# Kernel optimization log

Hardware: AMD Instinct MI355X
Metric: run time of the kernel (lower is better)

The kernel has to match this reference:

```python
import jax, jax.numpy as jnp
import numpy as np

BETA = 0.25

def setup_inputs() -> dict:
    key = jax.random.key(0)
    k1, k2 = jax.random.split(key)
    z_e = jax.random.normal(k1, (32768, 256), dtype=jnp.float32)
    codebook = jax.random.normal(k2, (8192, 256), dtype=jnp.float32)
    return {"z_e": z_e, "codebook": codebook}

def reference(z_e, codebook):
    # Squared distances via ||a||^2 - 2 a.b + ||b||^2 (argmin is invariant to sqrt)
    z_sq = jnp.sum(z_e * z_e, axis=1, keepdims=True)           # (B, 1)
    e_sq = jnp.sum(codebook * codebook, axis=1)                 # (K,)
    cross = jnp.einsum('bd,kd->bk', z_e, codebook)              # (B, K) GEMM
    d2 = z_sq - 2.0 * cross + e_sq[None, :]                     # (B, K)
    indices = jnp.argmin(d2, axis=1)                            # (B,)
    z_q = codebook[indices]                                     # (B, D)
    codebook_loss = jnp.mean((z_q - z_e) ** 2)
    commitment_loss = jnp.mean((z_e - z_q) ** 2)
    vq_loss = codebook_loss + BETA * commitment_loss
    # straight-through value (grad semantics irrelevant in fwd-only)
    z_q_st = z_e + (z_q - z_e)
    return (z_q_st, indices, vq_loss)
```

## Files before the change

kernel.cpp:

```cpp
#include <hip/hip_runtime.h>
#include <hip/hip_bf16.h>
#include <stdint.h>

#define M_ROWS 32768
#define N_CODES 8192
#define K_DIM 256
#define NSLICE 32
#define MARGIN 0.25f
#define MAXCAND 2560

#define BM 256
#define BN 256

typedef _Float16 half8 __attribute__((ext_vector_type(8)));
typedef float f4v __attribute__((ext_vector_type(4)));
typedef float f32x4 __attribute__((ext_vector_type(4)));
typedef __attribute__((address_space(3))) void lds_void;
typedef const __attribute__((address_space(1))) void gbl_cvoid;

__device__ __forceinline__ unsigned mono32(float f) {
    unsigned u = __float_as_uint(f);
    return (u & 0x80000000u) ? ~u : (u | 0x80000000u);
}
__device__ __forceinline__ unsigned long long pack_key(float d, unsigned col) {
    return ((unsigned long long)mono32(d) << 32) | (unsigned long long)col;
}
__device__ __forceinline__ float unpack_key(unsigned long long k) {
    unsigned m = (unsigned)(k >> 32);
    unsigned u = (m & 0x80000000u) ? (m & 0x7fffffffu) : ~m;
    return __uint_as_float(u);
}
__device__ __forceinline__ void merge2(unsigned long long& b1, unsigned long long& b2,
                                       unsigned long long o1, unsigned long long o2) {
    unsigned long long n1 = b1 < o1 ? b1 : o1;
    unsigned long long hi = b1 < o1 ? o1 : b1;
    unsigned long long l2 = b2 < o2 ? b2 : o2;
    b2 = hi < l2 ? hi : l2;
    b1 = n1;
}

__global__ __launch_bounds__(256) void prep_all(const float* __restrict__ z,
                                                const float* __restrict__ cb,
                                                _Float16* __restrict__ Aq,
                                                _Float16* __restrict__ Bq,
                                                float* __restrict__ esq) {
    int b = blockIdx.x;
    if (b < 5120) {
        const float* src = (b < 4096) ? z : cb;
        _Float16* dst = (b < 4096) ? Aq : Bq;
        int e = (b < 4096 ? b : b - 4096) * 256 + threadIdx.x;
        int ln = e & 63, kcg = (e >> 6) & 7, R = e >> 9;
        int row = R * 16 + (ln & 15);
        int k = kcg * 32 + (ln >> 4) * 8;
        const f4v* s4 = (const f4v*)(src + (size_t)row * K_DIM + k);
        f4v v0 = s4[0], v1 = s4[1];
        half8 h;
        #pragma unroll
        for (int j = 0; j < 4; ++j) h[j] = (_Float16)v0[j];
        #pragma unroll
        for (int j = 0; j < 4; ++j) h[4 + j] = (_Float16)v1[j];
        *(half8*)(dst + (size_t)e * 8) = h;
    } else {
        int wave = threadIdx.x >> 6, lane = threadIdx.x & 63;
        int row = (b - 5120) * 4 + wave;
        f4v v = *(const f4v*)(cb + (size_t)row * K_DIM + lane * 4);
        float sq = v[0] * v[0] + v[1] * v[1] + v[2] * v[2] + v[3] * v[3];
        #pragma unroll
        for (int m = 32; m; m >>= 1) sq += __shfl_xor(sq, m);
        if (lane == 0) esq[row] = sq;
    }
}

__global__ __launch_bounds__(512, 2) void coarse_gemm(
        const _Float16* __restrict__ Aq, const _Float16* __restrict__ Bq,
        const float* __restrict__ esq, ulonglong2* __restrict__ slices) {
    __shared__ __align__(16) char smem[131072];
    uint2 (*red)[4] = (uint2(*)[4])smem;

    int bid = blockIdx.x;
    int bn = bid & 31;
    int bm = bid >> 5;
    int m0 = bm * BM, n0 = bn * BN;

    int t = threadIdx.x;
    int lane = t & 63, wave = t >> 6;
    int l15 = lane & 15, quad = lane >> 4;
    int wr = wave >> 2, wc = wave & 3;

    float es_adj[4];
    #pragma unroll
    for (int ni = 0; ni < 4; ++ni)
        es_adj[ni] = esq[n0 + wc * 64 + ni * 16 + l15] + 1024.0f;
    asm volatile("" ::: "memory");

    f32x4 acc[8][4] = {};

    const char* Ab = (const char*)Aq + (size_t)bm * 131072;
    const char* Bb = (const char*)Bq + (size_t)bn * 131072;

    auto stage_half = [&](int ks, int op, int c, char* dstA, char* dstB) {
        const char* gb = op ? Bb : Ab;
        char* db = op ? dstB : dstA;
        #pragma unroll
        for (int i2 = 0; i2 < 2; ++i2) {
            int e = i2 * 512 + t;
            int RB = e >> 6, ln = e & 63;
            __builtin_amdgcn_global_load_lds(
                (gbl_cvoid*)(gb + ((size_t)(RB * 8 + ks * 2 + c) << 10) + ln * 16),
                (lds_void*)(db + ((RB * 2 + c) * 64 + ln) * 16), 16, 0, 0);
        }
    };

    {
        char* A0 = smem, * B0 = smem + 32768;
        stage_half(0, 0, 0, A0, B0);
        stage_half(0, 1, 0, A0, B0);
        stage_half(0, 0, 1, A0, B0);
        stage_half(0, 1, 1, A0, B0);
    }

    half8 bfr[4];
    #pragma unroll
    for (int j = 0; j < 4; ++j) {
        const char* As = smem + (j & 1) * 65536;
        const char* Bs = As + 32768;
        char* Asn = smem + ((j + 1) & 1) * 65536;
        char* Bsn = Asn + 32768;
        #pragma unroll
        for (int p = 0; p < 4; ++p) {
            const int c = p >> 1;
            const int mh = p & 1;
            if (p == 0 || p == 2) {
                if (j == 3 && p == 2)
                    asm volatile("s_waitcnt vmcnt(0)" ::: "memory");
                else
                    asm volatile("s_waitcnt vmcnt(4)" ::: "memory");
                __builtin_amdgcn_s_barrier();
                asm volatile("" ::: "memory");
            }
            half8 afr[4];
            #pragma unroll
            for (int mi = 0; mi < 4; ++mi) {
                int RB = wr * 8 + mh * 4 + mi;
                afr[mi] = *(const half8*)(As + ((RB * 2 + c) * 64 + lane) * 16);
            }
            if (mh == 0) {
                #pragma unroll
                for (int ni = 0; ni < 4; ++ni) {
                    int CB = wc * 4 + ni;
                    bfr[ni] = *(const half8*)(Bs + ((CB * 2 + c) * 64 + lane) * 16);
                }
            }
            if (j < 3) stage_half(j + 1, p & 1, p >> 1, Asn, Bsn);
            __builtin_amdgcn_s_barrier();
            asm volatile("s_waitcnt lgkmcnt(0)" ::: "memory");
            __builtin_amdgcn_sched_barrier(0);
            __builtin_amdgcn_s_setprio(1);
            #pragma unroll
            for (int mi = 0; mi < 4; ++mi)
                #pragma unroll
                for (int ni = 0; ni < 4; ++ni)
                    acc[mh * 4 + mi][ni] = __builtin_amdgcn_mfma_f32_16x16x32_f16(
                        afr[mi], bfr[ni], acc[mh * 4 + mi][ni], 0, 0, 0);
            __builtin_amdgcn_s_setprio(0);
        }
    }

    #pragma unroll
    for (int mi = 0; mi < 8; ++mi) {
        #pragma unroll
        for (int r = 0; r < 4; ++r) {
            unsigned b1 = 0xFFFFFFFFu, b2 = 0xFFFFFFFFu;
            #pragma unroll
            for (int ni = 0; ni < 4; ++ni) {
                float key = fmaf(-2.0f, acc[mi][ni][r], es_adj[ni]);
                unsigned kb = (__float_as_uint(key) & 0xFFFFFFC0u) |
                              (unsigned)(ni * 16 + l15);
                unsigned hi = kb > b1 ? kb : b1;
                b1 = kb < b1 ? kb : b1;
                b2 = hi < b2 ? hi : b2;
            }
            #pragma unroll
            for (int m = 1; m < 16; m <<= 1) {
                unsigned o1 = (unsigned)__shfl_xor((int)b1, m);
                unsigned o2 = (unsigned)__shfl_xor((int)b2, m);
                unsigned hi = b1 > o1 ? b1 : o1;
                b1 = b1 < o1 ? b1 : o1;
                unsigned l2 = b2 < o2 ? b2 : o2;
                b2 = hi < l2 ? hi : l2;
            }
            if (l15 == 0) {
                int rowl = wr * 128 + mi * 16 + quad * 4 + r;
                red[rowl][wc] = make_uint2(b1, b2);
            }
        }
    }
    __syncthreads();
    if (t < 256) {
        unsigned best = 0xFFFFFFFFu, sec = 0xFFFFFFFFu, bq = 0;
        #pragma unroll
        for (int q = 0; q < 4; ++q) {
            uint2 e = red[t][q];
            if (e.x < best) { sec = best; best = e.x; bq = (unsigned)q; }
            else sec = e.x < sec ? e.x : sec;
            sec = e.y < sec ? e.y : sec;
        }
        unsigned col = (unsigned)n0 + bq * 64u + (best & 63u);
        unsigned long long q1 =
            ((unsigned long long)((best & 0xFFFFFFC0u) | 0x80000000u) << 32) | col;
        unsigned long long q2 =
            ((unsigned long long)((sec & 0xFFFFFFC0u) | 0x80000000u) << 32) |
            0xFFFFFFFFull;
        slices[(size_t)(m0 + t) * NSLICE + bn] = make_ulonglong2(q1, q2);
    }
}

__global__ __launch_bounds__(256) void merge_slices(
        const ulonglong2* __restrict__ slices,
        int* __restrict__ bestidx, int* __restrict__ flags,
        int* __restrict__ list, int* __restrict__ count) {
    int t = threadIdx.x;
    int wave = t >> 6, lane = t & 63;
    int half = lane >> 5, idx = lane & 31;
    int row = blockIdx.x * 8 + wave * 2 + half;
    ulonglong2 p = slices[(size_t)row * NSLICE + idx];
    unsigned long long b1 = p.x, b2 = p.y;
    #pragma unroll
    for (int m = 1; m < 32; m <<= 1) {
        unsigned long long o1 = (unsigned long long)__shfl_xor((long long)b1, m);
        unsigned long long o2 = (unsigned long long)__shfl_xor((long long)b2, m);
        merge2(b1, b2, o1, o2);
    }
    if (idx == 0) {
        bestidx[row] = (int)(unsigned)(b1 & 0xFFFFFFFFULL);
        int f = (unpack_key(b2) - unpack_key(b1) <= MARGIN) ? 1 : 0;
        flags[row] = f;
        if (f) { int pos = atomicAdd(count, 1); list[pos] = row; }
    }
}

__global__ __launch_bounds__(256) void refine(
        const float* __restrict__ z, const float* __restrict__ cb,
        const ulonglong2* __restrict__ slices,
        const int* __restrict__ list, const int* __restrict__ count,
        int* __restrict__ bestidx) {
    __shared__ float zrow[K_DIM];
    __shared__ int cand[MAXCAND];
    __shared__ int ncand_s;
    __shared__ unsigned long long sb1;
    __shared__ double wd[4];
    __shared__ int wc[4];
    int t = threadIdx.x, lane = t & 63, wave = t >> 6;
    int n = *count;
    #pragma unroll 1
    for (int li = blockIdx.x; li < n; li += 2048) {
        int row = list[li];
        __syncthreads();
        zrow[t] = z[(size_t)row * K_DIM + t];
        if (t == 0) ncand_s = 0;
        __syncthreads();
        ulonglong2 p = make_ulonglong2(~0ULL, ~0ULL);
        if (wave == 0) {
            if (lane < NSLICE) p = slices[(size_t)row * NSLICE + lane];
            unsigned long long b1 = p.x;
            #pragma unroll
            for (int m = 1; m < 64; m <<= 1) {
                unsigned long long o =
                    (unsigned long long)__shfl_xor((long long)b1, m);
                b1 = o < b1 ? o : b1;
            }
            if (lane == 0) sb1 = b1;
        }
        __syncthreads();
        float thr = unpack_key(sb1) + MARGIN;
        if (wave == 0 && lane < NSLICE) {
            float k1 = unpack_key(p.x), k2 = unpack_key(p.y);
            if (k2 <= thr) {
                int pos = atomicAdd(&ncand_s, 256);
                if (pos + 256 <= MAXCAND)
                    for (int j = 0; j < 256; ++j) cand[pos + j] = lane * 256 + j;
            } else if (k1 <= thr) {
                int pos = atomicAdd(&ncand_s, 1);
                if (pos < MAXCAND) cand[pos] = (int)(unsigned)(p.x & 0xFFFFFFFFULL);
            }
        }
        __syncthreads();
        int nc = ncand_s;
        bool full = nc > MAXCAND;
        int total = full ? N_CODES : nc;
        double bd = 1e300;
        int bc = 0x7fffffff;
        #pragma unroll 1
        for (int base = 0; base < total; base += 256) {
            int i = base + t;
            if (i < total) {
                int code = full ? i : cand[i];
                const f4v* e4 = (const f4v*)(cb + (size_t)code * K_DIM);
                double s0 = 0, s1 = 0, s2 = 0, s3 = 0;
                #pragma unroll 4
                for (int k4 = 0; k4 < 64; ++k4) {
                    f4v e = e4[k4];
                    f4v zz = *(const f4v*)&zrow[k4 * 4];
                    float d0 = zz[0] - e[0], d1 = zz[1] - e[1];
                    float d2 = zz[2] - e[2], d3 = zz[3] - e[3];
                    s0 = fma((double)d0, (double)d0, s0);
                    s1 = fma((double)d1, (double)d1, s1);
                    s2 = fma((double)d2, (double)d2, s2);
                    s3 = fma((double)d3, (double)d3, s3);
                }
                double s = (s0 + s1) + (s2 + s3);
                if (s < bd || (s == bd && code < bc)) { bd = s; bc = code; }
            }
        }
        #pragma unroll
        for (int m = 1; m < 64; m <<= 1) {
            double od = __shfl_xor(bd, m);
            int oc = __shfl_xor(bc, m);
            if (od < bd || (od == bd && oc < bc)) { bd = od; bc = oc; }
        }
        if (lane == 0) { wd[wave] = bd; wc[wave] = bc; }
        __syncthreads();
        if (t == 0) {
            #pragma unroll
            for (int w = 1; w < 4; ++w)
                if (wd[w] < bd || (wd[w] == bd && wc[w] < bc)) { bd = wd[w]; bc = wc[w]; }
            bestidx[row] = bc;
        }
    }
}

__global__ __launch_bounds__(256) void vq_bruteforce(const float* __restrict__ z,
                                                     const float* __restrict__ cb,
                                                     float* __restrict__ out_idx) {
    __shared__ float As[128 * 16];
    __shared__ float Bs[128 * 16];
    int t = threadIdx.x;
    int tx = t & 15, ty = t >> 4;
    int r0 = blockIdx.x * 128;
    unsigned long long best[8];
    #pragma unroll
    for (int j = 0; j < 8; ++j) best[j] = ~0ULL;

    for (int n0 = 0; n0 < N_CODES; n0 += 128) {
        float acc[8][8] = {};
        for (int k0 = 0; k0 < K_DIM; k0 += 16) {
            __syncthreads();
            int row = t >> 1, c8 = (t & 1) * 8;
            #pragma unroll
            for (int j = 0; j < 8; ++j)
                As[row * 16 + c8 + j] = z[(size_t)(r0 + row) * K_DIM + k0 + c8 + j];
            #pragma unroll
            for (int j = 0; j < 8; ++j)
                Bs[row * 16 + c8 + j] = cb[(size_t)(n0 + row) * K_DIM + k0 + c8 + j];
            __syncthreads();
            #pragma unroll
            for (int k = 0; k < 16; ++k) {
                float a[8], b[8];
                #pragma unroll
                for (int j = 0; j < 8; ++j) a[j] = As[(ty * 8 + j) * 16 + k];
                #pragma unroll
                for (int j = 0; j < 8; ++j) b[j] = Bs[(tx * 8 + j) * 16 + k];
                #pragma unroll
                for (int i = 0; i < 8; ++i)
                    #pragma unroll
                    for (int j = 0; j < 8; ++j) {
                        float d = a[i] - b[j];
                        acc[i][j] += d * d;
                    }
            }
        }
        #pragma unroll
        for (int i = 0; i < 8; ++i) {
            unsigned long long bv = ~0ULL;
            #pragma unroll
            for (int j = 0; j < 8; ++j) {
                unsigned long long p =
                    pack_key(acc[i][j], (unsigned)(n0 + tx * 8 + j));
                bv = (p < bv) ? p : bv;
            }
            #pragma unroll
            for (int m = 1; m < 16; m <<= 1) {
                unsigned long long o =
                    (unsigned long long)__shfl_xor((long long)bv, m);
                bv = (o < bv) ? o : bv;
            }
            if (tx == 0 && bv < best[i]) best[i] = bv;
        }
    }
    if (tx == 0) {
        #pragma unroll
        for (int i = 0; i < 8; ++i)
            out_idx[r0 + ty * 8 + i] =
                (float)(unsigned)(best[i] & 0xFFFFFFFFULL);
    }
}

__global__ __launch_bounds__(256) void finalize(const float* __restrict__ z,
                                                const float* __restrict__ cb,
                                                const int* __restrict__ bestidx,
                                                float* __restrict__ out,
                                                double* __restrict__ accum,
                                                int use_int) {
    int wave = threadIdx.x >> 6, lane = threadIdx.x & 63;
    float* out_idx = out + (size_t)M_ROWS * K_DIM;
    float se = 0.f;
    #pragma unroll 1
    for (int row = blockIdx.x * 4 + wave; row < M_ROWS; row += 1024 * 4) {
        int idx = use_int ? bestidx[row] : (int)out_idx[row];
        f4v zv = *(const f4v*)(z  + (size_t)row * K_DIM + lane * 4);
        f4v qv = *(const f4v*)(cb + (size_t)idx * K_DIM + lane * 4);
        f4v ov;
        #pragma unroll
        for (int j = 0; j < 4; ++j) {
            float d = qv[j] - zv[j];
            ov[j] = zv[j] + d;
            se += d * d;
        }
        *(f4v*)(out + (size_t)row * K_DIM + lane * 4) = ov;
        if (lane == 0) out_idx[row] = (float)idx;
    }
    #pragma unroll
    for (int m = 32; m; m >>= 1) se += __shfl_xor(se, m);
    __shared__ float part[4];
    if (lane == 0) part[wave] = se;
    __syncthreads();
    if (threadIdx.x == 0)
        atomicAdd(accum, (double)((part[0] + part[1]) + (part[2] + part[3])));
}

__global__ void write_loss(const double* __restrict__ accum,
                           float* __restrict__ out) {
    out[(size_t)M_ROWS * K_DIM + M_ROWS] =
        (float)(1.25 * (*accum / (double)((size_t)M_ROWS * K_DIM)));
}

extern "C" void kernel_launch(void* const* d_in, const int* in_sizes, int n_in,
                              void* d_out, int out_size, void* d_ws, size_t ws_size,
                              hipStream_t stream) {
    const float* z  = (const float*)d_in[0];
    const float* cb = (const float*)d_in[1];
    float* out = (float*)d_out;
    float* out_idx = out + (size_t)M_ROWS * K_DIM;

    size_t offA  = 0;
    size_t offBq = offA + (size_t)M_ROWS * K_DIM * 2;
    size_t offE  = offBq + (size_t)N_CODES * K_DIM * 2;
    size_t offS  = offE + (size_t)N_CODES * 4;
    size_t offBI = offS + (size_t)M_ROWS * NSLICE * 16;
    size_t offF  = offBI + (size_t)M_ROWS * 4;
    size_t offL  = offF + (size_t)M_ROWS * 4;
    size_t offC  = offL + (size_t)M_ROWS * 4;
    size_t offAcc = offC + 16;
    size_t need  = offAcc + 16;

    if (ws_size >= need) {
        _Float16* Aq = (_Float16*)((char*)d_ws + offA);
        _Float16* Bq = (_Float16*)((char*)d_ws + offBq);
        float* esq   = (float*)((char*)d_ws + offE);
        ulonglong2* slices = (ulonglong2*)((char*)d_ws + offS);
        int* bestidx = (int*)((char*)d_ws + offBI);
        int* flags   = (int*)((char*)d_ws + offF);
        int* list    = (int*)((char*)d_ws + offL);
        int* count   = (int*)((char*)d_ws + offC);
        double* accum = (double*)((char*)d_ws + offAcc);

        hipMemsetAsync((char*)d_ws + offC, 0, 32, stream);

        prep_all<<<7168, 256, 0, stream>>>(z, cb, Aq, Bq, esq);
        coarse_gemm<<<(M_ROWS / BM) * (N_CODES / BN), 512, 0, stream>>>(
            Aq, Bq, esq, slices);
        merge_slices<<<M_ROWS / 8, 256, 0, stream>>>(slices, bestidx, flags,
                                                     list, count);
        refine<<<2048, 256, 0, stream>>>(z, cb, slices, list, count, bestidx);
        finalize<<<1024, 256, 0, stream>>>(z, cb, bestidx, out, accum, 1);
        write_loss<<<1, 1, 0, stream>>>(accum, out);
    } else {
        double* accum = (double*)d_ws;
        hipMemsetAsync(d_ws, 0, sizeof(double), stream);
        vq_bruteforce<<<M_ROWS / 128, 256, 0, stream>>>(z, cb, out_idx);
        finalize<<<1024, 256, 0, stream>>>(z, cb, nullptr, out, accum, 0);
        write_loss<<<1, 1, 0, stream>>>(accum, out);
    }
}
```

Before: 391.3 us.

## Keep A tile in registers and stream codebook through persistent coarse GEMM blocks

```diff
diff --git a/kernel.cpp b/kernel.cpp
--- a/kernel.cpp
+++ b/kernel.cpp
@@ -9,7 +9,7 @@
 #define MARGIN 0.25f
 #define MAXCAND 2560
 
-#define BM 256
+#define BM 128
 #define BN 256
 
 typedef _Float16 half8 __attribute__((ext_vector_type(8)));
@@ -74,144 +74,118 @@
 __global__ __launch_bounds__(512, 2) void coarse_gemm(
         const _Float16* __restrict__ Aq, const _Float16* __restrict__ Bq,
         const float* __restrict__ esq, ulonglong2* __restrict__ slices) {
-    __shared__ __align__(16) char smem[131072];
-    uint2 (*red)[4] = (uint2(*)[4])smem;
+    __shared__ __align__(16) char smem[36864];
+    uint2 (*red)[4] = (uint2(*)[4])(smem + 32768);
 
     int bid = blockIdx.x;
-    int bn = bid & 31;
-    int bm = bid >> 5;
-    int m0 = bm * BM, n0 = bn * BN;
+    int bm = bid >> 1, h = bid & 1;
+    int m0 = bm * BM;
 
     int t = threadIdx.x;
     int lane = t & 63, wave = t >> 6;
     int l15 = lane & 15, quad = lane >> 4;
     int wr = wave >> 2, wc = wave & 3;
 
-    float es_adj[4];
+    half8 aAll[8][4];
     #pragma unroll
-    for (int ni = 0; ni < 4; ++ni)
-        es_adj[ni] = esq[n0 + wc * 64 + ni * 16 + l15] + 1024.0f;
-    asm volatile("" ::: "memory");
-
-    f32x4 acc[8][4] = {};
-
-    const char* Ab = (const char*)Aq + (size_t)bm * 131072;
-    const char* Bb = (const char*)Bq + (size_t)bn * 131072;
-
-    auto stage_half = [&](int ks, int op, int c, char* dstA, char* dstB) {
-        const char* gb = op ? Bb : Ab;
-        char* db = op ? dstB : dstA;
-        #pragma unroll
-        for (int i2 = 0; i2 < 2; ++i2) {
-            int e = i2 * 512 + t;
-            int RB = e >> 6, ln = e & 63;
+    for (int kcg = 0; kcg < 8; ++kcg)
+        #pragma unroll
+        for (int mi = 0; mi < 4; ++mi)
+            aAll[kcg][mi] = *(const half8*)((const char*)Aq +
+                ((size_t)((bm * 8 + wr * 4 + mi) * 8 + kcg) << 10) + lane * 16);
+
+    const char* Bh = (const char*)Bq + (size_t)h * 16 * 131072;
+
+    auto stage = [&](int s) {
+        char* dst = smem + (s & 1) * 16384;
+        const char* src = Bh + ((size_t)(s >> 3) << 17);
+        int kc = s & 7;
+        #pragma unroll
+        for (int i = 0; i < 2; ++i) {
+            int e = i * 512 + t;
+            int CB = e >> 6, ln = e & 63;
             __builtin_amdgcn_global_load_lds(
-                (gbl_cvoid*)(gb + ((size_t)(RB * 8 + ks * 2 + c) << 10) + ln * 16),
-                (lds_void*)(db + ((RB * 2 + c) * 64 + ln) * 16), 16, 0, 0);
+                (gbl_cvoid*)(src + ((size_t)(CB * 8 + kc) << 10) + ln * 16),
+                (lds_void*)(dst + e * 16), 16, 0, 0);
         }
     };
 
-    {
-        char* A0 = smem, * B0 = smem + 32768;
-        stage_half(0, 0, 0, A0, B0);
-        stage_half(0, 1, 0, A0, B0);
-        stage_half(0, 0, 1, A0, B0);
-        stage_half(0, 1, 1, A0, B0);
-    }
-
-    half8 bfr[4];
-    #pragma unroll
-    for (int j = 0; j < 4; ++j) {
-        const char* As = smem + (j & 1) * 65536;
-        const char* Bs = As + 32768;
-        char* Asn = smem + ((j + 1) & 1) * 65536;
-        char* Bsn = Asn + 32768;
-        #pragma unroll
-        for (int p = 0; p < 4; ++p) {
-            const int c = p >> 1;
-            const int mh = p & 1;
-            if (p == 0 || p == 2) {
-                if (j == 3 && p == 2)
-                    asm volatile("s_waitcnt vmcnt(0)" ::: "memory");
-                else
-                    asm volatile("s_waitcnt vmcnt(4)" ::: "memory");
-                __builtin_amdgcn_s_barrier();
-                asm volatile("" ::: "memory");
-            }
-            half8 afr[4];
-            #pragma unroll
-            for (int mi = 0; mi < 4; ++mi) {
-                int RB = wr * 8 + mh * 4 + mi;
-                afr[mi] = *(const half8*)(As + ((RB * 2 + c) * 64 + lane) * 16);
-            }
-            if (mh == 0) {
+    stage(0);
+    __syncthreads();
+
+    #pragma unroll 1
+    for (int pn = 0; pn < 16; ++pn) {
+        f32x4 acc[4][4] = {};
+        #pragma unroll
+        for (int ks = 0; ks < 8; ++ks) {
+            int s = pn * 8 + ks;
+            if (s < 127) stage(s + 1);
+            const char* Bs = smem + (s & 1) * 16384;
+            half8 b[4];
+            #pragma unroll
+            for (int ni = 0; ni < 4; ++ni)
+                b[ni] = *(const half8*)(Bs + ((wc * 4 + ni) * 64 + lane) * 16);
+            #pragma unroll
+            for (int mi = 0; mi < 4; ++mi)
+                #pragma unroll
+                for (int ni = 0; ni < 4; ++ni)
+                    acc[mi][ni] = __builtin_amdgcn_mfma_f32_16x16x32_f16(
+                        aAll[ks][mi], b[ni], acc[mi][ni], 0, 0, 0);
+            __syncthreads();
+        }
+
+        int bn = h * 16 + pn, n0 = bn * BN;
+        float es_adj[4];
+        #pragma unroll
+        for (int ni = 0; ni < 4; ++ni)
+            es_adj[ni] = esq[n0 + wc * 64 + ni * 16 + l15] + 1024.0f;
+
+        #pragma unroll
+        for (int mi = 0; mi < 4; ++mi) {
+            #pragma unroll
+            for (int r = 0; r < 4; ++r) {
+                unsigned b1 = 0xFFFFFFFFu, b2 = 0xFFFFFFFFu;
                 #pragma unroll
                 for (int ni = 0; ni < 4; ++ni) {
-                    int CB = wc * 4 + ni;
-                    bfr[ni] = *(const half8*)(Bs + ((CB * 2 + c) * 64 + lane) * 16);
+                    float key = fmaf(-2.0f, acc[mi][ni][r], es_adj[ni]);
+                    unsigned kb = (__float_as_uint(key) & 0xFFFFFFC0u) |
+                                  (unsigned)(ni * 16 + l15);
+                    unsigned hi2 = kb > b1 ? kb : b1;
+                    b1 = kb < b1 ? kb : b1;
+                    b2 = hi2 < b2 ? hi2 : b2;
                 }
-            }
-            if (j < 3) stage_half(j + 1, p & 1, p >> 1, Asn, Bsn);
-            __builtin_amdgcn_s_barrier();
-            asm volatile("s_waitcnt lgkmcnt(0)" ::: "memory");
-            __builtin_amdgcn_sched_barrier(0);
-            __builtin_amdgcn_s_setprio(1);
-            #pragma unroll
-            for (int mi = 0; mi < 4; ++mi)
-                #pragma unroll
-                for (int ni = 0; ni < 4; ++ni)
-                    acc[mh * 4 + mi][ni] = __builtin_amdgcn_mfma_f32_16x16x32_f16(
-                        afr[mi], bfr[ni], acc[mh * 4 + mi][ni], 0, 0, 0);
-            __builtin_amdgcn_s_setprio(0);
-        }
-    }
-
-    #pragma unroll
-    for (int mi = 0; mi < 8; ++mi) {
-        #pragma unroll
-        for (int r = 0; r < 4; ++r) {
-            unsigned b1 = 0xFFFFFFFFu, b2 = 0xFFFFFFFFu;
-            #pragma unroll
-            for (int ni = 0; ni < 4; ++ni) {
-                float key = fmaf(-2.0f, acc[mi][ni][r], es_adj[ni]);
-                unsigned kb = (__float_as_uint(key) & 0xFFFFFFC0u) |
-                              (unsigned)(ni * 16 + l15);
-                unsigned hi = kb > b1 ? kb : b1;
-                b1 = kb < b1 ? kb : b1;
-                b2 = hi < b2 ? hi : b2;
-            }
-            #pragma unroll
-            for (int m = 1; m < 16; m <<= 1) {
-                unsigned o1 = (unsigned)__shfl_xor((int)b1, m);
-                unsigned o2 = (unsigned)__shfl_xor((int)b2, m);
-                unsigned hi = b1 > o1 ? b1 : o1;
-                b1 = b1 < o1 ? b1 : o1;
-                unsigned l2 = b2 < o2 ? b2 : o2;
-                b2 = hi < l2 ? hi : l2;
-            }
-            if (l15 == 0) {
-                int rowl = wr * 128 + mi * 16 + quad * 4 + r;
-                red[rowl][wc] = make_uint2(b1, b2);
-            }
-        }
-    }
-    __syncthreads();
-    if (t < 256) {
-        unsigned best = 0xFFFFFFFFu, sec = 0xFFFFFFFFu, bq = 0;
-        #pragma unroll
-        for (int q = 0; q < 4; ++q) {
-            uint2 e = red[t][q];
-            if (e.x < best) { sec = best; best = e.x; bq = (unsigned)q; }
-            else sec = e.x < sec ? e.x : sec;
-            sec = e.y < sec ? e.y : sec;
-        }
-        unsigned col = (unsigned)n0 + bq * 64u + (best & 63u);
-        unsigned long long q1 =
-            ((unsigned long long)((best & 0xFFFFFFC0u) | 0x80000000u) << 32) | col;
-        unsigned long long q2 =
-            ((unsigned long long)((sec & 0xFFFFFFC0u) | 0x80000000u) << 32) |
-            0xFFFFFFFFull;
-        slices[(size_t)(m0 + t) * NSLICE + bn] = make_ulonglong2(q1, q2);
+                #pragma unroll
+                for (int m = 1; m < 16; m <<= 1) {
+                    unsigned o1 = (unsigned)__shfl_xor((int)b1, m);
+                    unsigned o2 = (unsigned)__shfl_xor((int)b2, m);
+                    unsigned hi2 = b1 > o1 ? b1 : o1;
+                    b1 = b1 < o1 ? b1 : o1;
+                    unsigned l2 = b2 < o2 ? b2 : o2;
+                    b2 = hi2 < l2 ? hi2 : l2;
+                }
+                if (l15 == 0)
+                    red[wr * 64 + mi * 16 + quad * 4 + r][wc] =
+                        make_uint2(b1, b2);
+            }
+        }
+        __syncthreads();
+        if (t < 128) {
+            unsigned best = 0xFFFFFFFFu, sec = 0xFFFFFFFFu, bq = 0;
+            #pragma unroll
+            for (int q = 0; q < 4; ++q) {
+                uint2 e = red[t][q];
+                if (e.x < best) { sec = best; best = e.x; bq = (unsigned)q; }
+                else sec = e.x < sec ? e.x : sec;
+                sec = e.y < sec ? e.y : sec;
+            }
+            unsigned col = (unsigned)n0 + bq * 64u + (best & 63u);
+            unsigned long long q1 =
+                ((unsigned long long)((best & 0xFFFFFFC0u) | 0x80000000u) << 32) | col;
+            unsigned long long q2 =
+                ((unsigned long long)((sec & 0xFFFFFFC0u) | 0x80000000u) << 32) |
+                0xFFFFFFFFull;
+            slices[(size_t)(m0 + t) * NSLICE + bn] = make_ulonglong2(q1, q2);
+        }
     }
 }
 
@@ -232,7 +206,7 @@
         merge2(b1, b2, o1, o2);
     }
     if (idx == 0) {
-        bestidx[row] = (int)(unsigned)(b1 & 0xFFFFFFFFULL);
+        bestidx[row] = (int)((unsigned)b1 & (N_CODES - 1));
         int f = (unpack_key(b2) - unpack_key(b1) <= MARGIN) ? 1 : 0;
         flags[row] = f;
         if (f) { int pos = atomicAdd(count, 1); list[pos] = row; }
@@ -281,7 +255,8 @@
                     for (int j = 0; j < 256; ++j) cand[pos + j] = lane * 256 + j;
             } else if (k1 <= thr) {
                 int pos = atomicAdd(&ncand_s, 1);
-                if (pos < MAXCAND) cand[pos] = (int)(unsigned)(p.x & 0xFFFFFFFFULL);
+                if (pos < MAXCAND)
+                    cand[pos] = (int)((unsigned)p.x & (N_CODES - 1));
             }
         }
         __syncthreads();
@@ -407,6 +382,7 @@
     #pragma unroll 1
     for (int row = blockIdx.x * 4 + wave; row < M_ROWS; row += 1024 * 4) {
         int idx = use_int ? bestidx[row] : (int)out_idx[row];
+        idx &= (N_CODES - 1);
         f4v zv = *(const f4v*)(z  + (size_t)row * K_DIM + lane * 4);
         f4v qv = *(const f4v*)(cb + (size_t)idx * K_DIM + lane * 4);
         f4v ov;
@@ -467,7 +443,7 @@
         hipMemsetAsync((char*)d_ws + offC, 0, 32, stream);
 
         prep_all<<<7168, 256, 0, stream>>>(z, cb, Aq, Bq, esq);
-        coarse_gemm<<<(M_ROWS / BM) * (N_CODES / BN), 512, 0, stream>>>(
+        coarse_gemm<<<(M_ROWS / BM) * 2, 512, 0, stream>>>(
             Aq, Bq, esq, slices);
         merge_slices<<<M_ROWS / 8, 256, 0, stream>>>(slices, bestidx, flags,
                                                      list, count);
```

After: 423.9 us. 8.3% more time.
